# Optimization experiments

Measured on AMD Instinct MI355X. Metric: run time of the kernel, lower is better.

The kernel has to match this reference:

```python
import jax, jax.numpy as jnp
import numpy as np

N_NODES = 100000
IN_F, HID_F, OUT_F = 128, 128, 64
N_EDGES = 1600000


def _gcn_conv(x, src, dst, n, W, b):
    # x: [N, Fin]; src/dst: [E'] (self-loops already appended)
    h = x @ W                                        # [N, Fout]
    deg = jax.ops.segment_sum(jnp.ones_like(dst, dtype=h.dtype), dst,
                              num_segments=n)        # in-degree incl. self-loop
    dinv = jnp.where(deg > 0, jax.lax.rsqrt(deg), 0.0)
    norm = dinv[src] * dinv[dst]                     # [E']
    msg = h[src] * norm[:, None]                     # [E', Fout] gather + scale
    out = jax.ops.segment_sum(msg, dst, num_segments=n)
    return out + b


def setup_inputs() -> dict:
    key = jax.random.key(0)
    ks = jax.random.split(key, 6)
    x = jax.random.normal(ks[0], (N_NODES, IN_F), dtype=jnp.float32)
    edge_index = jax.random.randint(ks[1], (2, N_EDGES), 0, N_NODES, dtype=jnp.int64)
    # Glorot-ish init for weights, zeros for biases (PyG GCNConv default)
    W1 = jax.random.normal(ks[2], (IN_F, HID_F), dtype=jnp.float32) / np.sqrt(IN_F)
    b1 = jnp.zeros((HID_F,), dtype=jnp.float32)
    W2 = jax.random.normal(ks[3], (HID_F, OUT_F), dtype=jnp.float32) / np.sqrt(HID_F)
    b2 = jnp.zeros((OUT_F,), dtype=jnp.float32)
    return {"x": x, "edge_index": edge_index, "W1": W1, "b1": b1, "W2": W2, "b2": b2}


def reference(x, edge_index, W1, b1, W2, b2):
    n = x.shape[0]
    # GCNConv adds self-loops, then symmetric deg^-1/2 normalization
    loops = jnp.arange(n, dtype=edge_index.dtype)
    src = jnp.concatenate([edge_index[0], loops])
    dst = jnp.concatenate([edge_index[1], loops])
    h = _gcn_conv(x, src, dst, n, W1, b1)
    h = jax.nn.relu(h)
    out = _gcn_conv(h, src, dst, n, W2, b2)
    return out
```

## Files before the change

kernel.cpp:

```cpp
#include <hip/hip_runtime.h>
#include <hip/hip_fp16.h>

#define N_NODES 100000
#define N_EDGES 1600000
#define BNODES  128
#define NBUCK   782
#define CAP     3072
#define BIN_TILE 8192
#define BIN_BLOCKS 196
#define LDSK    136


typedef _Float16 half8 __attribute__((ext_vector_type(8)));
typedef float    f32x4 __attribute__((ext_vector_type(4)));

__device__ __forceinline__ float bcf(float v, int l) {
    return __int_as_float(__builtin_amdgcn_readlane(__float_as_int(v), l));
}


__global__ __launch_bounds__(1024, 1) void k_bin(const int* __restrict__ src,
                                                 const int* __restrict__ dst,
                                                 int* __restrict__ cursor,
                                                 unsigned int* __restrict__ staged) {
    __shared__ unsigned int stg[BIN_TILE];
    __shared__ unsigned short stgb[BIN_TILE];
    __shared__ int hist[NBUCK];
    __shared__ int lbase[NBUCK];
    __shared__ int gbs[NBUCK];
    __shared__ int wsum[16];

    int t = threadIdx.x;
    int lane = t & 63, wv = t >> 6;
    long base = (long)blockIdx.x * BIN_TILE;
    int nval = (int)min((long)BIN_TILE, (long)N_EDGES - base);

    for (int i = t; i < NBUCK; i += 1024) hist[i] = 0;
    __syncthreads();

    unsigned int ent[8], brk[8];
#pragma unroll
    for (int r = 0; r < 8; r++) {
        int i = r * 1024 + t;
        if (i < nval) {
            int s = src[base + i], d = dst[base + i];
            int b = d >> 7;
            int rk = atomicAdd(&hist[b], 1);
            ent[r] = ((unsigned int)(d & 127) << 17) | (unsigned int)s;
            brk[r] = ((unsigned int)b << 16) | (unsigned int)rk;
        } else {
            brk[r] = 0xFFFFFFFFu;
        }
    }
    __syncthreads();

    {
        int v = (t < NBUCK) ? hist[t] : 0;
        int x = v;
#pragma unroll
        for (int o = 1; o < 64; o <<= 1) {
            int u = __shfl_up(x, o);
            if (lane >= o) x += u;
        }
        if (lane == 63) wsum[wv] = x;
        __syncthreads();
        if (wv == 0) {
            int ws = (lane < 16) ? wsum[lane] : 0;
#pragma unroll
            for (int o = 1; o < 16; o <<= 1) {
                int u = __shfl_up(ws, o);
                if (lane >= o) ws += u;
            }
            if (lane < 16) wsum[lane] = ws;
        }
        __syncthreads();
        int incl = x + (wv > 0 ? wsum[wv - 1] : 0);
        if (t < NBUCK) lbase[t] = incl - v;
    }
    __syncthreads();

#pragma unroll
    for (int r = 0; r < 8; r++) {
        if (brk[r] != 0xFFFFFFFFu) {
            int b  = (int)(brk[r] >> 16);
            int rk = (int)(brk[r] & 0xFFFF);
            int p  = lbase[b] + rk;
            stg[p]  = ent[r];
            stgb[p] = (unsigned short)b;
        }
    }
    __syncthreads();

    if (t < NBUCK) gbs[t] = (hist[t] > 0) ? atomicAdd(&cursor[t], hist[t]) : 0;
    __syncthreads();

    for (int i = t; i < nval; i += 1024) {
        int b = stgb[i];
        int pos = gbs[b] + (i - lbase[b]);
        if (pos < CAP) staged[(size_t)b * CAP + pos] = stg[i];
    }
}


__global__ __launch_bounds__(512) void k_fill3(const unsigned int* __restrict__ staged,
                                               const int* __restrict__ cursor,
                                               int* __restrict__ col,
                                               int2* __restrict__ rpse,
                                               float* __restrict__ dinv) {
    __shared__ int stg[CAP];
    __shared__ int lcnt[BNODES];
    __shared__ int lbase[BNODES];
    __shared__ int lpos[BNODES];
    __shared__ int sscan[BNODES];

    int b = blockIdx.x, t = threadIdx.x;
    int n = min(cursor[b], CAP);
    const unsigned int* sp = staged + (size_t)b * CAP;

    if (t < BNODES) lcnt[t] = 0;
    __syncthreads();

    unsigned int ent[CAP / 512];
#pragma unroll
    for (int r = 0; r < CAP / 512; r++) {
        int i = r * 512 + t;
        if (i < n) {
            ent[r] = sp[i];
            atomicAdd(&lcnt[ent[r] >> 17], 1);
        }
    }
    __syncthreads();

    if (t < BNODES) sscan[t] = lcnt[t];
    __syncthreads();
    for (int o = 1; o < BNODES; o <<= 1) {
        int u = (t < BNODES && t >= o) ? sscan[t - o] : 0;
        __syncthreads();
        if (t < BNODES) sscan[t] += u;
        __syncthreads();
    }
    if (t < BNODES) {
        int ex = sscan[t] - lcnt[t];
        lbase[t] = ex;
        lpos[t]  = ex;
        int node = b * BNODES + t;
        if (node < N_NODES) {
            dinv[node] = rsqrtf((float)(lcnt[t] + 1));
            rpse[node] = make_int2(b * CAP + ex, b * CAP + ex + lcnt[t]);
        }
    }
    __syncthreads();

#pragma unroll
    for (int r = 0; r < CAP / 512; r++) {
        int i = r * 512 + t;
        if (i < n) {
            int dl = (int)(ent[r] >> 17);
            int pos = atomicAdd(&lpos[dl], 1);
            stg[pos] = (int)(ent[r] & 0x1FFFFu);
        }
    }
    __syncthreads();

    for (int i = t; i < n; i += 512) col[(size_t)b * CAP + i] = stg[i];
}


template <int NOUT, bool F32IN>
__global__ __launch_bounds__(256) void k_gemm_mfma(const void* __restrict__ Xv,
                                                   const float* __restrict__ W,
                                                   __half* __restrict__ H) {
    __shared__ _Float16 wt[NOUT * LDSK];
    for (int idx = threadIdx.x; idx < 64 * NOUT; idx += 256) {
        int kp = idx / NOUT;
        int n  = idx - kp * NOUT;
        __half2 p = __floats2half2_rn(W[(2 * kp) * NOUT + n], W[(2 * kp + 1) * NOUT + n]);
        *reinterpret_cast<__half2*>(&wt[n * LDSK + 2 * kp]) = p;
    }
    __syncthreads();

    int wv = threadIdx.x >> 6, l = threadIdx.x & 63;
    int m = l & 15, g = l >> 4;
    int row0 = blockIdx.x * 64 + wv * 16;
    int lrow = min(row0 + m, N_NODES - 1);

    f32x4 acc[NOUT / 16];
#pragma unroll
    for (int c = 0; c < NOUT / 16; c++) acc[c] = (f32x4){0.f, 0.f, 0.f, 0.f};

#pragma unroll
    for (int kk = 0; kk < 4; kk++) {
        int k0 = kk * 32 + g * 8;
        half8 a;
        if (F32IN) {
            const float* xp = (const float*)Xv + (size_t)lrow * 128 + k0;
#pragma unroll
            for (int j = 0; j < 8; j++) a[j] = (_Float16)xp[j];
        } else {
            a = *reinterpret_cast<const half8*>((const _Float16*)Xv + (size_t)lrow * 128 + k0);
        }
#pragma unroll
        for (int c = 0; c < NOUT / 16; c++) {
            half8 b = *reinterpret_cast<const half8*>(&wt[(c * 16 + m) * LDSK + k0]);
            acc[c] = __builtin_amdgcn_mfma_f32_16x16x32_f16(a, b, acc[c], 0, 0, 0);
        }
    }

#pragma unroll
    for (int c = 0; c < NOUT / 16; c++)
#pragma unroll
        for (int r = 0; r < 4; r++) {
            int grow = row0 + g * 4 + r;
            if (grow < N_NODES)
                H[(size_t)grow * NOUT + c * 16 + m] = __float2half(acc[c][r]);
        }
}


__global__ __launch_bounds__(256) void k_agg1(const _Float16* __restrict__ H1,
                                              const float* __restrict__ dinv,
                                              const int2* __restrict__ rpse,
                                              const int* __restrict__ col,
                                              const float* __restrict__ b1,
                                              __half2* __restrict__ H2) {
    int node = blockIdx.x * 4 + (threadIdx.x >> 6);
    int lane = threadIdx.x & 63;
    int k = lane & 31, h = lane >> 5;

    float di = dinv[node];
    int2 se = rpse[node];
    int e0 = se.x, e1 = se.y;

    float a0 = 0.f, a1 = 0.f, a2 = 0.f, a3 = 0.f;

    for (int cb = e0; cb < e1; cb += 64) {
        int n = min(64, e1 - cb);
        int idx = cb + lane;
        int cv = col[idx < e1 ? idx : e0];
        float wf = dinv[cv] * di;

        for (int j = 0; j < n; j += 16) {
            float2 v[8];
            float  w[8];
#pragma unroll
            for (int q = 0; q < 8; q++) {
                if (j + 2 * q < n) {
                    int e  = j + 2 * q + h;
                    int es = e < n ? e : (n - 1);
                    int   s  = __shfl(cv, es);
                    float ww = __shfl(wf, es);
                    w[q] = (e < n) ? ww : 0.f;
                    v[q] = reinterpret_cast<const float2*>(H1 + (size_t)s * 128)[k];
                } else {
                    w[q] = 0.f;
                    v[q] = make_float2(0.f, 0.f);
                }
            }
#pragma unroll
            for (int q = 0; q < 8; q++) {
                __half2 pa = *reinterpret_cast<__half2*>(&v[q].x);
                __half2 pb = *reinterpret_cast<__half2*>(&v[q].y);
                float2 fa = __half22float2(pa), fb = __half22float2(pb);
                a0 += fa.x * w[q];
                a1 += fa.y * w[q];
                a2 += fb.x * w[q];
                a3 += fb.y * w[q];
            }
        }
    }

    a0 += __shfl_xor(a0, 32);
    a1 += __shfl_xor(a1, 32);
    a2 += __shfl_xor(a2, 32);
    a3 += __shfl_xor(a3, 32);

    float s0 = h ? a2 : a0;
    float s1 = h ? a3 : a1;
    const __half2* H1v = reinterpret_cast<const __half2*>(H1);
    float2 sv = __half22float2(H1v[(size_t)node * 64 + 2 * k + h]);
    s0 = fmaxf(s0 + sv.x * di * di + b1[4 * k + 2 * h], 0.f);
    s1 = fmaxf(s1 + sv.y * di * di + b1[4 * k + 2 * h + 1], 0.f);
    H2[(size_t)node * 64 + 2 * k + h] = __floats2half2_rn(s0, s1);
}


__global__ __launch_bounds__(256) void k_agg2(const _Float16* __restrict__ H3,
                                              const float* __restrict__ dinv,
                                              const int2* __restrict__ rpse,
                                              const int* __restrict__ col,
                                              const float* __restrict__ b2,
                                              float* __restrict__ out) {
    int node = (blockIdx.x * 256 + threadIdx.x) >> 6;
    int lane = threadIdx.x & 63;
    if (node >= N_NODES) return;
    int k = lane & 15, q4 = lane >> 4;

    float di = dinv[node];
    int2 se = rpse[node];
    int e0 = se.x, e1 = se.y;

    float a0 = 0.f, a1 = 0.f, a2 = 0.f, a3 = 0.f;

    for (int cb = e0; cb < e1; cb += 64) {
        int n = min(64, e1 - cb);
        int idx = cb + lane;
        int cv = col[idx < e1 ? idx : e0];
        float wf = dinv[cv] * di;

        for (int j = 0; j < n; j += 32) {
            float2 v[8];
            float  w[8];
#pragma unroll
            for (int q = 0; q < 8; q++) {
                if (j + 4 * q < n) {
                    int e  = j + 4 * q + q4;
                    int es = e < n ? e : (n - 1);
                    int   s  = __shfl(cv, es);
                    float ww = __shfl(wf, es);
                    w[q] = (e < n) ? ww : 0.f;
                    v[q] = reinterpret_cast<const float2*>(H3 + (size_t)s * 64)[k];
                } else {
                    w[q] = 0.f;
                    v[q] = make_float2(0.f, 0.f);
                }
            }
#pragma unroll
            for (int q = 0; q < 8; q++) {
                __half2 pa = *reinterpret_cast<__half2*>(&v[q].x);
                __half2 pb = *reinterpret_cast<__half2*>(&v[q].y);
                float2 fa = __half22float2(pa), fb = __half22float2(pb);
                a0 += fa.x * w[q];
                a1 += fa.y * w[q];
                a2 += fb.x * w[q];
                a3 += fb.y * w[q];
            }
        }
    }

    a0 += __shfl_xor(a0, 16); a1 += __shfl_xor(a1, 16);
    a2 += __shfl_xor(a2, 16); a3 += __shfl_xor(a3, 16);
    a0 += __shfl_xor(a0, 32); a1 += __shfl_xor(a1, 32);
    a2 += __shfl_xor(a2, 32); a3 += __shfl_xor(a3, 32);

    if (lane < 32) {
        int hh = lane >> 4;
        float s0 = hh ? a2 : a0;
        float s1 = hh ? a3 : a1;
        const __half2* H3v = reinterpret_cast<const __half2*>(H3);
        float2 sv = __half22float2(H3v[(size_t)node * 32 + 2 * k + hh]);
        s0 += sv.x * di * di + b2[4 * k + 2 * hh];
        s1 += sv.y * di * di + b2[4 * k + 2 * hh + 1];
        float2 r{s0, s1};
        *reinterpret_cast<float2*>(out + (size_t)node * 64 + 4 * k + 2 * hh) = r;
    }
}


extern "C" void kernel_launch(void* const* d_in, const int* in_sizes, int n_in,
                              void* d_out, int out_size, void* d_ws, size_t ws_size,
                              hipStream_t stream) {
    const float* x  = (const float*)d_in[0];
    const int*   ei = (const int*)d_in[1];
    const float* W1 = (const float*)d_in[2];
    const float* b1 = (const float*)d_in[3];
    const float* W2 = (const float*)d_in[4];
    const float* b2 = (const float*)d_in[5];
    float* out = (float*)d_out;

    const int* src = ei;
    const int* dst = ei + N_EDGES;

    char* ws = (char*)d_ws;
    size_t off = 0;
    auto alloc = [&](size_t bytes) -> void* {
        off = (off + 255) & ~(size_t)255;
        void* p = ws + off;
        off += bytes;
        return p;
    };
    int*          cursor = (int*)alloc((size_t)NBUCK * 4);
    float*        dinv   = (float*)alloc((size_t)N_NODES * 4);
    int2*         rpse   = (int2*)alloc((size_t)N_NODES * 8);
    unsigned int* staged = (unsigned int*)alloc((size_t)NBUCK * CAP * 4);
    int*          col    = (int*)alloc((size_t)NBUCK * CAP * 4);
    _Float16*     h1     = (_Float16*)alloc((size_t)N_NODES * 128 * 2);
    _Float16*     h2     = (_Float16*)alloc((size_t)N_NODES * 128 * 2);
    _Float16*     h3     = (_Float16*)alloc((size_t)N_NODES * 64 * 2);

    hipMemsetAsync(cursor, 0, (size_t)NBUCK * 4, stream);

    k_bin<<<BIN_BLOCKS, 1024, 0, stream>>>(src, dst, cursor, staged);
    k_fill3<<<NBUCK, 512, 0, stream>>>(staged, cursor, col, rpse, dinv);

    int gblk = (N_NODES + 63) / 64;

    k_gemm_mfma<128, true><<<gblk, 256, 0, stream>>>(x, W1, (__half*)h1);
    k_agg1<<<N_NODES / 4, 256, 0, stream>>>(h1, dinv, rpse, col, b1, (__half2*)h2);

    k_gemm_mfma<64, false><<<gblk, 256, 0, stream>>>(h2, W2, (__half*)h3);
    k_agg2<<<(N_NODES * 64 + 255) / 256, 256, 0, stream>>>(h3, dinv, rpse, col, b2, out);
}
```

Measured before the change: 181.6 us.

## Slice layer-1 features into 16-wide column panels for cache-local aggregation

The first GEMM now writes H1 in a feature-sliced layout of eight panels, each N_NODES×16 halfs, and the second GEMM reads H2 in the same layout. The layer-1 aggregation becomes one kernel with 8× more blocks, each block handling a single 16-feature slice. Each panel is about 3.2 MB, so the random neighbour gathers should stay cache-resident. In exchange, the edge list and dinv are re-read eight times, each gather is only 4 bytes per lane, and the reduction needs extra shuffles. Column loads are marked nontemporal.

Result: slower. 401.5 us (+121.1%).

```diff
diff --git a/kernel.cpp b/kernel.cpp
--- a/kernel.cpp
+++ b/kernel.cpp
@@ -166,7 +166,7 @@
 }
 
 
-template <int NOUT, bool F32IN>
+template <int NOUT, bool F32IN, bool ASLICE, bool DSLICE>
 __global__ __launch_bounds__(256) void k_gemm_mfma(const void* __restrict__ Xv,
                                                    const float* __restrict__ W,
                                                    __half* __restrict__ H) {
@@ -192,7 +192,11 @@
     for (int kk = 0; kk < 4; kk++) {
         int k0 = kk * 32 + g * 8;
         half8 a;
-        if (F32IN) {
+        if constexpr (ASLICE) {
+            const _Float16* ap = (const _Float16*)Xv +
+                ((size_t)(k0 >> 4) * N_NODES + lrow) * 16 + (k0 & 15);
+            a = *reinterpret_cast<const half8*>(ap);
+        } else if constexpr (F32IN) {
             const float* xp = (const float*)Xv + (size_t)lrow * 128 + k0;
 #pragma unroll
             for (int j = 0; j < 8; j++) a[j] = (_Float16)xp[j];
@@ -211,76 +215,65 @@
 #pragma unroll
         for (int r = 0; r < 4; r++) {
             int grow = row0 + g * 4 + r;
-            if (grow < N_NODES)
-                H[(size_t)grow * NOUT + c * 16 + m] = __float2half(acc[c][r]);
-        }
-}
-
-
-__global__ __launch_bounds__(256) void k_agg1(const _Float16* __restrict__ H1,
-                                              const float* __restrict__ dinv,
-                                              const int2* __restrict__ rpse,
-                                              const int* __restrict__ col,
-                                              const float* __restrict__ b1,
-                                              __half2* __restrict__ H2) {
-    int node = blockIdx.x * 4 + (threadIdx.x >> 6);
+            if (grow < N_NODES) {
+                if constexpr (DSLICE)
+                    H[((size_t)c * N_NODES + grow) * 16 + m] = __float2half(acc[c][r]);
+                else
+                    H[(size_t)grow * NOUT + c * 16 + m] = __float2half(acc[c][r]);
+            }
+        }
+}
+
+
+__global__ __launch_bounds__(256) void k_agg1s(const _Float16* __restrict__ H1,
+                                               const float* __restrict__ dinv,
+                                               const int2* __restrict__ rpse,
+                                               const int* __restrict__ col,
+                                               const float* __restrict__ b1,
+                                               __half2* __restrict__ H2) {
+    int fs = blockIdx.x & 7, nb = blockIdx.x >> 3;
+    int node = nb * 4 + (threadIdx.x >> 6);
     int lane = threadIdx.x & 63;
-    int k = lane & 31, h = lane >> 5;
+    int k = lane & 7, g8 = lane >> 3;
+
+    const _Float16* Hs = H1 + (size_t)fs * N_NODES * 16;
 
     float di = dinv[node];
     int2 se = rpse[node];
     int e0 = se.x, e1 = se.y;
 
-    float a0 = 0.f, a1 = 0.f, a2 = 0.f, a3 = 0.f;
+    float a0 = 0.f, a1 = 0.f;
 
     for (int cb = e0; cb < e1; cb += 64) {
         int n = min(64, e1 - cb);
         int idx = cb + lane;
-        int cv = col[idx < e1 ? idx : e0];
+        int cv = __builtin_nontemporal_load(&col[idx < e1 ? idx : e0]);
         float wf = dinv[cv] * di;
 
-        for (int j = 0; j < n; j += 16) {
-            float2 v[8];
-            float  w[8];
-#pragma unroll
-            for (int q = 0; q < 8; q++) {
-                if (j + 2 * q < n) {
-                    int e  = j + 2 * q + h;
-                    int es = e < n ? e : (n - 1);
-                    int   s  = __shfl(cv, es);
-                    float ww = __shfl(wf, es);
-                    w[q] = (e < n) ? ww : 0.f;
-                    v[q] = reinterpret_cast<const float2*>(H1 + (size_t)s * 128)[k];
-                } else {
-                    w[q] = 0.f;
-                    v[q] = make_float2(0.f, 0.f);
-                }
-            }
-#pragma unroll
-            for (int q = 0; q < 8; q++) {
-                __half2 pa = *reinterpret_cast<__half2*>(&v[q].x);
-                __half2 pb = *reinterpret_cast<__half2*>(&v[q].y);
-                float2 fa = __half22float2(pa), fb = __half22float2(pb);
-                a0 += fa.x * w[q];
-                a1 += fa.y * w[q];
-                a2 += fb.x * w[q];
-                a3 += fb.y * w[q];
-            }
-        }
-    }
-
-    a0 += __shfl_xor(a0, 32);
-    a1 += __shfl_xor(a1, 32);
-    a2 += __shfl_xor(a2, 32);
-    a3 += __shfl_xor(a3, 32);
-
-    float s0 = h ? a2 : a0;
-    float s1 = h ? a3 : a1;
-    const __half2* H1v = reinterpret_cast<const __half2*>(H1);
-    float2 sv = __half22float2(H1v[(size_t)node * 64 + 2 * k + h]);
-    s0 = fmaxf(s0 + sv.x * di * di + b1[4 * k + 2 * h], 0.f);
-    s1 = fmaxf(s1 + sv.y * di * di + b1[4 * k + 2 * h + 1], 0.f);
-    H2[(size_t)node * 64 + 2 * k + h] = __floats2half2_rn(s0, s1);
+        for (int j = 0; j < n; j += 8) {
+            int e  = j + g8;
+            int es = e < n ? e : (n - 1);
+            int   s  = __shfl(cv, es);
+            float ww = __shfl(wf, es);
+            float w  = (e < n) ? ww : 0.f;
+            float v = *reinterpret_cast<const float*>(Hs + (size_t)s * 16 + 2 * k);
+            float2 f = __half22float2(*reinterpret_cast<__half2*>(&v));
+            a0 += f.x * w;
+            a1 += f.y * w;
+        }
+    }
+
+    a0 += __shfl_xor(a0, 8);  a1 += __shfl_xor(a1, 8);
+    a0 += __shfl_xor(a0, 16); a1 += __shfl_xor(a1, 16);
+    a0 += __shfl_xor(a0, 32); a1 += __shfl_xor(a1, 32);
+
+    if (g8 == 0) {
+        float vs = *reinterpret_cast<const float*>(Hs + (size_t)node * 16 + 2 * k);
+        float2 sv = __half22float2(*reinterpret_cast<__half2*>(&vs));
+        float s0 = fmaxf(a0 + sv.x * di * di + b1[fs * 16 + 2 * k], 0.f);
+        float s1 = fmaxf(a1 + sv.y * di * di + b1[fs * 16 + 2 * k + 1], 0.f);
+        H2[((size_t)fs * N_NODES + node) * 8 + k] = __floats2half2_rn(s0, s1);
+    }
 }
 
 
@@ -394,9 +387,10 @@
 
     int gblk = (N_NODES + 63) / 64;
 
-    k_gemm_mfma<128, true><<<gblk, 256, 0, stream>>>(x, W1, (__half*)h1);
-    k_agg1<<<N_NODES / 4, 256, 0, stream>>>(h1, dinv, rpse, col, b1, (__half2*)h2);
-
-    k_gemm_mfma<64, false><<<gblk, 256, 0, stream>>>(h2, W2, (__half*)h3);
+    k_gemm_mfma<128, true, false, true><<<gblk, 256, 0, stream>>>(x, W1, (__half*)h1);
+    k_agg1s<<<(N_NODES / 4) * 8, 256, 0, stream>>>(h1, dinv, rpse, col, b1,
+                                                   (__half2*)h2);
+
+    k_gemm_mfma<64, false, true, false><<<gblk, 256, 0, stream>>>(h2, W2, (__half*)h3);
     k_agg2<<<(N_NODES * 64 + 255) / 256, 256, 0, stream>>>(h3, dinv, rpse, col, b2, out);
 }
```
